# Kernel tuning notes

Hardware: AMD Instinct MI355X
Metric: run time of the kernel (lower is better)

Reference implementation:

```python
import jax, jax.numpy as jnp
import numpy as np


def setup_inputs() -> dict:
    key = jax.random.key(0)
    k1, k2, k3, k4, k5 = jax.random.split(key, 5)
    N, E, C_in, C_out = 100000, 1600000, 64, 64
    x = jax.random.normal(k1, (N, C_in), dtype=jnp.float32)
    edge_index = jax.random.randint(k2, (2, E), 0, N, dtype=jnp.int64)
    edge_weight = jax.random.uniform(k3, (E,), dtype=jnp.float32)
    # Xavier-uniform Linear weights [out, in], zero biases (matches reset_parameters)
    bound = float(np.sqrt(6.0 / (C_in + C_out)))
    W_self = jax.random.uniform(k4, (C_out, C_in), dtype=jnp.float32, minval=-bound, maxval=bound)
    W_neigh = jax.random.uniform(k5, (C_out, C_in), dtype=jnp.float32, minval=-bound, maxval=bound)
    b_self = jnp.zeros((C_out,), dtype=jnp.float32)
    b_neigh = jnp.zeros((C_out,), dtype=jnp.float32)
    return {"x": x, "edge_index": edge_index, "edge_weight": edge_weight,
            "W_self": W_self, "b_self": b_self, "W_neigh": W_neigh, "b_neigh": b_neigh,
            "num_nodes": N}


def reference(x, edge_index, edge_weight, W_self, b_self, W_neigh, b_neigh, num_nodes):
    row, col = edge_index[0], edge_index[1]
    # gather source features, weight, scatter-add to destinations: [E, C] -> [N, C]
    message = x[col] * edge_weight[:, None]
    neigh_agg = jax.ops.segment_sum(message, row, num_segments=num_nodes)
    # two linear projections (torch Linear: y = x @ W.T + b)
    return x @ W_self.T + b_self + neigh_agg @ W_neigh.T + b_neigh
```

## Files before the change

### kernel.cpp

```cpp
#include <hip/hip_runtime.h>
#include <hip/hip_bf16.h>


#define C 64
#define BKT 128
#define MAXB 800
#define BINT 6144
#define BTHR 1024
#define CAP 2560

typedef __attribute__((ext_vector_type(8))) short bf16x8;
typedef __attribute__((ext_vector_type(4))) float f32x4;

__device__ inline unsigned short f2bf(float f) {
    union { __hip_bfloat16 h; unsigned short u; } c;
    c.h = __float2bfloat16(f);
    return c.u;
}

__device__ inline float bflo16(unsigned int u) {
    return __int_as_float((int)(u << 16));
}
__device__ inline float bfhi16(unsigned int u) {
    return __int_as_float((int)(u & 0xFFFF0000u));
}

__global__ __launch_bounds__(256) void prep_kernel(
        const int* __restrict__ ei, int* __restrict__ bhist, int E, int NBK,
        const float* __restrict__ x, unsigned short* __restrict__ xb, int n4,
        const float* __restrict__ Ws, const float* __restrict__ Wn,
        unsigned short* __restrict__ Wsb, unsigned short* __restrict__ Wnb) {
    __shared__ int lh[MAXB];
    const int t = threadIdx.x;
    for (int i = t; i < NBK; i += 256) lh[i] = 0;
    __syncthreads();
    const int gtid = blockIdx.x * 256 + t;
    const int gs = gridDim.x * 256;
    for (int e = gtid; e < E; e += gs)
        atomicAdd(&lh[ei[e] >> 7], 1);
    __syncthreads();
    for (int i = t; i < NBK; i += 256)
        if (lh[i]) atomicAdd(&bhist[i], lh[i]);
    const float4* x4 = (const float4*)x;
    ushort4* xb4 = (ushort4*)xb;
    for (int i = gtid; i < n4; i += gs) {
        float4 v = x4[i];
        ushort4 o;
        o.x = f2bf(v.x); o.y = f2bf(v.y); o.z = f2bf(v.z); o.w = f2bf(v.w);
        xb4[i] = o;
    }
    if (gtid < 1024) {
        float4 v = ((const float4*)Ws)[gtid];
        ushort4 o;
        o.x = f2bf(v.x); o.y = f2bf(v.y); o.z = f2bf(v.z); o.w = f2bf(v.w);
        ((ushort4*)Wsb)[gtid] = o;
        v = ((const float4*)Wn)[gtid];
        o.x = f2bf(v.x); o.y = f2bf(v.y); o.z = f2bf(v.z); o.w = f2bf(v.w);
        ((ushort4*)Wnb)[gtid] = o;
    }
}

__global__ __launch_bounds__(1024) void scan_kernel(
        const int* __restrict__ bhist, int* __restrict__ boffs,
        int* __restrict__ bcur, int NBK) {
    __shared__ int s[1024];
    const int t = threadIdx.x;
    s[t] = (t < NBK) ? bhist[t] : 0;
    __syncthreads();
    for (int off = 1; off < 1024; off <<= 1) {
        int v = 0;
        if (t >= off) v = s[t - off];
        __syncthreads();
        if (t >= off) s[t] += v;
        __syncthreads();
    }
    if (t < NBK) {
        int e = (t > 0) ? s[t - 1] : 0;
        boffs[t] = e;
        bcur[t] = e;
        if (t == NBK - 1) boffs[NBK] = s[t];
    }
}

__global__ __launch_bounds__(BTHR) void bin_kernel(
        const int* __restrict__ ei, const float* __restrict__ ew,
        int* __restrict__ bcur, const int* __restrict__ unused,
        int2* __restrict__ sorted, int E, int NBK) {
    __shared__ int2 stage[BINT];
    __shared__ unsigned short stageb[BINT];
    __shared__ int h[MAXB];
    __shared__ int cur[MAXB];
    __shared__ int adj[MAXB];
    __shared__ int wsum[16];

    const int t = threadIdx.x;
    const int lane = t & 63;
    const int wv = t >> 6;
    const int e0 = blockIdx.x * BINT;
    const int cnt = min(BINT, E - e0);

    for (int i = t; i < NBK; i += BTHR) h[i] = 0;
    __syncthreads();

#pragma unroll
    for (int k = 0; k < BINT / BTHR; ++k) {
        const int idx = t + k * BTHR;
        if (idx < cnt) atomicAdd(&h[ei[e0 + idx] >> 7], 1);
    }
    __syncthreads();

    const int val = (t < NBK) ? h[t] : 0;
    int v = val;
#pragma unroll
    for (int off = 1; off < 64; off <<= 1) {
        const int u = __shfl_up(v, off);
        if (lane >= off) v += u;
    }
    if (lane == 63) wsum[wv] = v;
    __syncthreads();
    if (t < 64) {
        int s = (lane < 16) ? wsum[lane] : 0;
#pragma unroll
        for (int off = 1; off < 16; off <<= 1) {
            const int u = __shfl_up(s, off);
            if (lane >= off) s += u;
        }
        if (lane < 16) wsum[lane] = s;
    }
    __syncthreads();
    if (t < NBK) {
        const int incl = v + ((wv > 0) ? wsum[wv - 1] : 0);
        const int excl = incl - val;
        cur[t] = excl;
        const int g = val ? atomicAdd(&bcur[t], val) : 0;
        adj[t] = g - excl;
    }
    __syncthreads();

#pragma unroll
    for (int k = 0; k < BINT / BTHR; ++k) {
        const int idx = t + k * BTHR;
        if (idx < cnt) {
            const int e = e0 + idx;
            const int d = ei[e];
            const int s = ei[E + e];
            const float w = ew[e];
            const int b = d >> 7;
            const int dl = d & 127;
            const int p = atomicAdd(&cur[b], 1);
            stage[p] = make_int2((dl << 17) | s, __float_as_int(w));
            stageb[p] = (unsigned short)b;
        }
    }
    __syncthreads();

    for (int i = t; i < cnt; i += BTHR) {
        const int b = stageb[i];
        sorted[adj[b] + i] = stage[i];
    }
}

__global__ __launch_bounds__(512) void agg_kernel(
        const unsigned short* __restrict__ xb,
        const int2* __restrict__ sorted,
        const int* __restrict__ boffs,
        float* __restrict__ agg,
        unsigned short* __restrict__ aggb,
        int N) {
    __shared__ int2 meta2[CAP];
    __shared__ int lcnt[BKT];
    __shared__ int lincl[BKT];
    __shared__ int lcur[BKT];

    const int t = threadIdx.x;
    const int b = blockIdx.x;
    const int node0 = b << 7;
    const int lane = t & 63;
    const int wv = t >> 6;
    const int oct = lane >> 3;
    const int co = lane & 7;

    const bool h1 = (lane & 8) != 0;
    const bool h2 = (lane & 16) != 0;
    const bool h3 = (lane & 32) != 0;
    const int ch = co * 8 + (h1 ? 4 : 0) + (h2 ? 2 : 0) + (h3 ? 1 : 0);

    const uint4* xb8 = (const uint4*)xb;

    const int beg = boffs[b];
    const int end = boffs[b + 1];

    int chunk = beg;
    do {
        const int cc = (end - chunk < CAP) ? (end - chunk) : CAP;

        for (int i = t; i < BKT; i += 512) lcnt[i] = 0;
        __syncthreads();

        for (int i = t; i < cc; i += 512)
            atomicAdd(&lcnt[sorted[chunk + i].x >> 17], 1);
        __syncthreads();

        if (t < BKT) lincl[t] = lcnt[t];
        __syncthreads();
        for (int off = 1; off < BKT; off <<= 1) {
            int v = 0;
            if (t < BKT && t >= off) v = lincl[t - off];
            __syncthreads();
            if (t < BKT && t >= off) lincl[t] += v;
            __syncthreads();
        }
        if (t < BKT) lcur[t] = lincl[t] - lcnt[t];
        __syncthreads();

        for (int i = t; i < cc; i += 512) {
            const int2 m = sorted[chunk + i];
            const int dl = m.x >> 17;
            const int p = atomicAdd(&lcur[dl], 1);
            meta2[p] = make_int2(m.x & 0x1FFFF, m.y);
        }
        __syncthreads();

        const bool first = (chunk == beg);
        const bool last = (chunk + CAP >= end);

        for (int r = wv; r < BKT; r += 8) {
            const int s1 = lincl[r];
            const int s0 = s1 - lcnt[r];
            float a0 = 0.f, a1 = 0.f, a2 = 0.f, a3 = 0.f;
            float a4 = 0.f, a5 = 0.f, a6 = 0.f, a7 = 0.f;
            int j = s0 + oct;
            for (; j + 8 < s1; j += 16) {
                const int2 m0 = meta2[j];
                const int2 m1 = meta2[j + 8];
                const uint4 u0 = xb8[(unsigned)m0.x * 8u + co];
                const uint4 u1 = xb8[(unsigned)m1.x * 8u + co];
                const float w0 = __int_as_float(m0.y);
                const float w1 = __int_as_float(m1.y);
                a0 += w0 * bflo16(u0.x); a1 += w0 * bfhi16(u0.x);
                a2 += w0 * bflo16(u0.y); a3 += w0 * bfhi16(u0.y);
                a4 += w0 * bflo16(u0.z); a5 += w0 * bfhi16(u0.z);
                a6 += w0 * bflo16(u0.w); a7 += w0 * bfhi16(u0.w);
                a0 += w1 * bflo16(u1.x); a1 += w1 * bfhi16(u1.x);
                a2 += w1 * bflo16(u1.y); a3 += w1 * bfhi16(u1.y);
                a4 += w1 * bflo16(u1.z); a5 += w1 * bfhi16(u1.z);
                a6 += w1 * bflo16(u1.w); a7 += w1 * bfhi16(u1.w);
            }
            if (j < s1) {
                const int2 m0 = meta2[j];
                const uint4 u0 = xb8[(unsigned)m0.x * 8u + co];
                const float w0 = __int_as_float(m0.y);
                a0 += w0 * bflo16(u0.x); a1 += w0 * bfhi16(u0.x);
                a2 += w0 * bflo16(u0.y); a3 += w0 * bfhi16(u0.y);
                a4 += w0 * bflo16(u0.z); a5 += w0 * bfhi16(u0.z);
                a6 += w0 * bflo16(u0.w); a7 += w0 * bfhi16(u0.w);
            }
            float r0 = __shfl_xor(h1 ? a0 : a4, 8);
            float r1 = __shfl_xor(h1 ? a1 : a5, 8);
            float r2 = __shfl_xor(h1 ? a2 : a6, 8);
            float r3 = __shfl_xor(h1 ? a3 : a7, 8);
            const float b0 = (h1 ? a4 : a0) + r0;
            const float b1 = (h1 ? a5 : a1) + r1;
            const float b2 = (h1 ? a6 : a2) + r2;
            const float b3 = (h1 ? a7 : a3) + r3;
            float r4 = __shfl_xor(h2 ? b0 : b2, 16);
            float r5 = __shfl_xor(h2 ? b1 : b3, 16);
            const float c0 = (h2 ? b2 : b0) + r4;
            const float c1 = (h2 ? b3 : b1) + r5;
            float r6 = __shfl_xor(h3 ? c0 : c1, 32);
            float vfin = (h3 ? c1 : c0) + r6;

            const int node = node0 + r;
            if (node < N) {
                const size_t off = (size_t)node * C + ch;
                if (last) {
                    if (!first) vfin += agg[off];
                    aggb[off] = f2bf(vfin);
                } else {
                    if (first) agg[off] = vfin;
                    else       agg[off] += vfin;
                }
            }
        }
        chunk += CAP;
        __syncthreads();
    } while (chunk < end);
}

__global__ __launch_bounds__(256) void scatter_kernel(
        const float* __restrict__ x, const int* __restrict__ ei,
        const float* __restrict__ ew, float* __restrict__ agg, int E) {
    const int lane = threadIdx.x & 63;
    const int wid = (blockIdx.x * blockDim.x + threadIdx.x) >> 6;
    const int nw = (gridDim.x * blockDim.x) >> 6;
    for (int base = wid * 64; base < E; base += nw * 64) {
        const int e = base + lane;
        int dst = 0, src = 0; float w = 0.f;
        if (e < E) { dst = ei[e]; src = ei[E + e]; w = ew[e]; }
        const int cnt = min(64, E - base);
        for (int j = 0; j < cnt; ++j) {
            const int d = __shfl(dst, j);
            const int s = __shfl(src, j);
            const float wj = __shfl(w, j);
            atomicAdd(&agg[d * C + lane], x[s * C + lane] * wj);
        }
    }
}

__device__ inline bf16x8 cvt8(const float* __restrict__ p) {
    f32x4 lo = *(const f32x4*)p;
    f32x4 hi = *(const f32x4*)(p + 4);
    union { bf16x8 v; __hip_bfloat16 e[8]; } u;
#pragma unroll
    for (int j = 0; j < 4; ++j) u.e[j] = __float2bfloat16(lo[j]);
#pragma unroll
    for (int j = 0; j < 4; ++j) u.e[4 + j] = __float2bfloat16(hi[j]);
    return u.v;
}

__global__ __launch_bounds__(256) void proj_kernel(
        const float* __restrict__ x, const float* __restrict__ agg,
        const float* __restrict__ Ws, const float* __restrict__ bs,
        const float* __restrict__ Wn, const float* __restrict__ bn,
        float* __restrict__ out, int N) {
    const int lane = threadIdx.x & 63;
    const int wid = (blockIdx.x * blockDim.x + threadIdx.x) >> 6;
    const int l15 = lane & 15;
    const int quad = lane >> 4;
    const int nTiles = N >> 4;
    if (wid >= nTiles) return;
    const int m0 = wid << 4;

    bf16x8 bsf[4][2], bnf[4][2];
#pragma unroll
    for (int tt = 0; tt < 4; ++tt) {
        const int o = tt * 16 + l15;
#pragma unroll
        for (int h = 0; h < 2; ++h) {
            bsf[tt][h] = cvt8(Ws + o * C + h * 32 + quad * 8);
            bnf[tt][h] = cvt8(Wn + o * C + h * 32 + quad * 8);
        }
    }

    const int m = m0 + l15;
    bf16x8 ax[2], ag[2];
#pragma unroll
    for (int h = 0; h < 2; ++h) {
        ax[h] = cvt8(x + m * C + h * 32 + quad * 8);
        ag[h] = cvt8(agg + m * C + h * 32 + quad * 8);
    }

#pragma unroll
    for (int tt = 0; tt < 4; ++tt) {
        f32x4 acc = {0.f, 0.f, 0.f, 0.f};
        acc = __builtin_amdgcn_mfma_f32_16x16x32_bf16(ax[0], bsf[tt][0], acc, 0, 0, 0);
        acc = __builtin_amdgcn_mfma_f32_16x16x32_bf16(ax[1], bsf[tt][1], acc, 0, 0, 0);
        acc = __builtin_amdgcn_mfma_f32_16x16x32_bf16(ag[0], bnf[tt][0], acc, 0, 0, 0);
        acc = __builtin_amdgcn_mfma_f32_16x16x32_bf16(ag[1], bnf[tt][1], acc, 0, 0, 0);
        const int o = tt * 16 + l15;
        const float bias = bs[o] + bn[o];
#pragma unroll
        for (int r = 0; r < 4; ++r)
            out[(m0 + quad * 4 + r) * C + o] = acc[r] + bias;
    }
}

__global__ __launch_bounds__(256) void projb_kernel(
        const unsigned short* __restrict__ xb,
        const unsigned short* __restrict__ aggb,
        const unsigned short* __restrict__ Wsb, const float* __restrict__ bs,
        const unsigned short* __restrict__ Wnb, const float* __restrict__ bn,
        float* __restrict__ out, int N) {
    const int lane = threadIdx.x & 63;
    const int wid = (blockIdx.x * blockDim.x + threadIdx.x) >> 6;
    const int l15 = lane & 15;
    const int quad = lane >> 4;
    const int nTiles = N >> 4;
    if (wid >= nTiles) return;
    const int m0 = wid << 4;

    bf16x8 bsf[4][2], bnf[4][2];
#pragma unroll
    for (int tt = 0; tt < 4; ++tt) {
        const int o = tt * 16 + l15;
#pragma unroll
        for (int h = 0; h < 2; ++h) {
            bsf[tt][h] = *(const bf16x8*)(Wsb + o * C + h * 32 + quad * 8);
            bnf[tt][h] = *(const bf16x8*)(Wnb + o * C + h * 32 + quad * 8);
        }
    }

    const int m = m0 + l15;
    bf16x8 ax[2], ag[2];
#pragma unroll
    for (int h = 0; h < 2; ++h) {
        ax[h] = *(const bf16x8*)(xb + (size_t)m * C + h * 32 + quad * 8);
        ag[h] = *(const bf16x8*)(aggb + (size_t)m * C + h * 32 + quad * 8);
    }

#pragma unroll
    for (int tt = 0; tt < 4; ++tt) {
        f32x4 acc = {0.f, 0.f, 0.f, 0.f};
        acc = __builtin_amdgcn_mfma_f32_16x16x32_bf16(ax[0], bsf[tt][0], acc, 0, 0, 0);
        acc = __builtin_amdgcn_mfma_f32_16x16x32_bf16(ax[1], bsf[tt][1], acc, 0, 0, 0);
        acc = __builtin_amdgcn_mfma_f32_16x16x32_bf16(ag[0], bnf[tt][0], acc, 0, 0, 0);
        acc = __builtin_amdgcn_mfma_f32_16x16x32_bf16(ag[1], bnf[tt][1], acc, 0, 0, 0);
        const int o = tt * 16 + l15;
        const float bias = bs[o] + bn[o];
#pragma unroll
        for (int r = 0; r < 4; ++r)
            out[(m0 + quad * 4 + r) * C + o] = acc[r] + bias;
    }
}

extern "C" void kernel_launch(void* const* d_in, const int* in_sizes, int n_in,
                              void* d_out, int out_size, void* d_ws, size_t ws_size,
                              hipStream_t stream) {
    const float* x  = (const float*)d_in[0];
    const int*   ei = (const int*)d_in[1];
    const float* ew = (const float*)d_in[2];
    const float* Ws = (const float*)d_in[3];
    const float* bs = (const float*)d_in[4];
    const float* Wn = (const float*)d_in[5];
    const float* bn = (const float*)d_in[6];

    const int N = in_sizes[0] / C;
    const int E = in_sizes[2];
    const int NBK = (N + BKT - 1) / BKT;

    char* p = (char*)d_ws;
    float* agg = (float*)p;                  p += (size_t)N * C * sizeof(float);
    unsigned short* xb = (unsigned short*)p;  p += (size_t)N * C * sizeof(short);
    unsigned short* aggb = (unsigned short*)p; p += (size_t)N * C * sizeof(short);
    int2* sorted = (int2*)p;                 p += (size_t)E * sizeof(int2);
    unsigned short* Wsb = (unsigned short*)p; p += (size_t)C * C * sizeof(short);
    unsigned short* Wnb = (unsigned short*)p; p += (size_t)C * C * sizeof(short);
    int* bhist = (int*)p;                    p += (size_t)MAXB * sizeof(int);
    int* boffs = (int*)p;                    p += (size_t)(MAXB + 1) * sizeof(int);
    int* bcur = (int*)p;                     p += (size_t)MAXB * sizeof(int);
    const size_t needed = (size_t)(p - (char*)d_ws);

    const int nTiles = N / 16;
    const int projBlocks = (nTiles + 3) / 4;

    if (needed <= ws_size && N <= (1 << 17) && NBK <= MAXB) {
        const int n4 = N * C / 4;
        hipMemsetAsync(bhist, 0, (size_t)NBK * sizeof(int), stream);
        prep_kernel<<<1024, 256, 0, stream>>>(ei, bhist, E, NBK, x, xb, n4,
                                              Ws, Wn, Wsb, Wnb);
        scan_kernel<<<1, 1024, 0, stream>>>(bhist, boffs, bcur, NBK);
        bin_kernel<<<(E + BINT - 1) / BINT, BTHR, 0, stream>>>(ei, ew, bcur, bhist,
                                                               sorted, E, NBK);
        agg_kernel<<<NBK, 512, 0, stream>>>(xb, sorted, boffs, agg, aggb, N);
        projb_kernel<<<projBlocks, 256, 0, stream>>>(xb, aggb, Wsb, bs, Wnb, bn,
                                                     (float*)d_out, N);
    } else {
        hipMemsetAsync(agg, 0, (size_t)N * C * sizeof(float), stream);
        scatter_kernel<<<2048, 256, 0, stream>>>(x, ei, ew, agg, E);
        proj_kernel<<<projBlocks, 256, 0, stream>>>(x, agg, Ws, bs, Wn, bn,
                                                    (float*)d_out, N);
    }
}
```

Measured before the change: 194.5 us.

## Fuse projection into aggregation kernel and move bf16 conversion into bin kernel

The projection GEMM now runs inside agg_kernel: each block writes its aggregated bf16 rows into a swizzled LDS tile and applies MFMA projections directly. This drops the aggb buffer round trip and one kernel launch. The x/weight bf16 conversion moves from prep_kernel to the tail of bin_kernel, and the agg per-chunk scan uses wave shuffles instead of a barrier-heavy LDS scan. The extra 16KB LDS tile may lower agg_kernel occupancy, and weights are now read from global memory per tile.

```diff
diff --git a/kernel.cpp b/kernel.cpp
--- a/kernel.cpp
+++ b/kernel.cpp
@@ -26,10 +26,7 @@
 }
 
 __global__ __launch_bounds__(256) void prep_kernel(
-        const int* __restrict__ ei, int* __restrict__ bhist, int E, int NBK,
-        const float* __restrict__ x, unsigned short* __restrict__ xb, int n4,
-        const float* __restrict__ Ws, const float* __restrict__ Wn,
-        unsigned short* __restrict__ Wsb, unsigned short* __restrict__ Wnb) {
+        const int* __restrict__ ei, int* __restrict__ bhist, int E, int NBK) {
     __shared__ int lh[MAXB];
     const int t = threadIdx.x;
     for (int i = t; i < NBK; i += 256) lh[i] = 0;
@@ -41,23 +38,6 @@
     __syncthreads();
     for (int i = t; i < NBK; i += 256)
         if (lh[i]) atomicAdd(&bhist[i], lh[i]);
-    const float4* x4 = (const float4*)x;
-    ushort4* xb4 = (ushort4*)xb;
-    for (int i = gtid; i < n4; i += gs) {
-        float4 v = x4[i];
-        ushort4 o;
-        o.x = f2bf(v.x); o.y = f2bf(v.y); o.z = f2bf(v.z); o.w = f2bf(v.w);
-        xb4[i] = o;
-    }
-    if (gtid < 1024) {
-        float4 v = ((const float4*)Ws)[gtid];
-        ushort4 o;
-        o.x = f2bf(v.x); o.y = f2bf(v.y); o.z = f2bf(v.z); o.w = f2bf(v.w);
-        ((ushort4*)Wsb)[gtid] = o;
-        v = ((const float4*)Wn)[gtid];
-        o.x = f2bf(v.x); o.y = f2bf(v.y); o.z = f2bf(v.z); o.w = f2bf(v.w);
-        ((ushort4*)Wnb)[gtid] = o;
-    }
 }
 
 __global__ __launch_bounds__(1024) void scan_kernel(
@@ -84,8 +64,11 @@
 
 __global__ __launch_bounds__(BTHR) void bin_kernel(
         const int* __restrict__ ei, const float* __restrict__ ew,
-        int* __restrict__ bcur, const int* __restrict__ unused,
-        int2* __restrict__ sorted, int E, int NBK) {
+        int* __restrict__ bcur,
+        int2* __restrict__ sorted, int E, int NBK,
+        const float* __restrict__ x, unsigned short* __restrict__ xb, int n4,
+        const float* __restrict__ Ws, const float* __restrict__ Wn,
+        unsigned short* __restrict__ Wsb, unsigned short* __restrict__ Wnb) {
     __shared__ int2 stage[BINT];
     __shared__ unsigned short stageb[BINT];
     __shared__ int h[MAXB];
@@ -158,6 +141,26 @@
         const int b = stageb[i];
         sorted[adj[b] + i] = stage[i];
     }
+
+    const int gtid = blockIdx.x * BTHR + t;
+    const int gs = gridDim.x * BTHR;
+    const float4* x4 = (const float4*)x;
+    ushort4* xb4 = (ushort4*)xb;
+    for (int i = gtid; i < n4; i += gs) {
+        float4 vv = x4[i];
+        ushort4 o;
+        o.x = f2bf(vv.x); o.y = f2bf(vv.y); o.z = f2bf(vv.z); o.w = f2bf(vv.w);
+        xb4[i] = o;
+    }
+    if (gtid < 1024) {
+        float4 vv = ((const float4*)Ws)[gtid];
+        ushort4 o;
+        o.x = f2bf(vv.x); o.y = f2bf(vv.y); o.z = f2bf(vv.z); o.w = f2bf(vv.w);
+        ((ushort4*)Wsb)[gtid] = o;
+        vv = ((const float4*)Wn)[gtid];
+        o.x = f2bf(vv.x); o.y = f2bf(vv.y); o.z = f2bf(vv.z); o.w = f2bf(vv.w);
+        ((ushort4*)Wnb)[gtid] = o;
+    }
 }
 
 __global__ __launch_bounds__(512) void agg_kernel(
@@ -165,12 +168,14 @@
         const int2* __restrict__ sorted,
         const int* __restrict__ boffs,
         float* __restrict__ agg,
-        unsigned short* __restrict__ aggb,
-        int N) {
+        const unsigned short* __restrict__ Wsb, const float* __restrict__ bs,
+        const unsigned short* __restrict__ Wnb, const float* __restrict__ bn,
+        float* __restrict__ out, int N) {
     __shared__ int2 meta2[CAP];
     __shared__ int lcnt[BKT];
     __shared__ int lincl[BKT];
     __shared__ int lcur[BKT];
+    __shared__ unsigned short tile[BKT * C];
 
     const int t = threadIdx.x;
     const int b = blockIdx.x;
@@ -179,6 +184,8 @@
     const int wv = t >> 6;
     const int oct = lane >> 3;
     const int co = lane & 7;
+    const int l15 = lane & 15;
+    const int quad = lane >> 4;
 
     const bool h1 = (lane & 8) != 0;
     const bool h2 = (lane & 16) != 0;
@@ -201,15 +208,19 @@
             atomicAdd(&lcnt[sorted[chunk + i].x >> 17], 1);
         __syncthreads();
 
-        if (t < BKT) lincl[t] = lcnt[t];
-        __syncthreads();
-        for (int off = 1; off < BKT; off <<= 1) {
-            int v = 0;
-            if (t < BKT && t >= off) v = lincl[t - off];
-            __syncthreads();
-            if (t < BKT && t >= off) lincl[t] += v;
-            __syncthreads();
-        }
+        if (t < BKT) {
+            int sv = lcnt[t];
+            int acc = sv;
+#pragma unroll
+            for (int off = 1; off < 64; off <<= 1) {
+                const int u = __shfl_up(acc, off);
+                if (lane >= off) acc += u;
+            }
+            lincl[t] = acc;
+        }
+        __syncthreads();
+        if (t >= 64 && t < BKT) lincl[t] += lincl[63];
+        __syncthreads();
         if (t < BKT) lcur[t] = lincl[t] - lcnt[t];
         __syncthreads();
 
@@ -271,17 +282,53 @@
             float vfin = (h3 ? c1 : c0) + r6;
 
             const int node = node0 + r;
-            if (node < N) {
-                const size_t off = (size_t)node * C + ch;
-                if (last) {
-                    if (!first) vfin += agg[off];
-                    aggb[off] = f2bf(vfin);
-                } else {
-                    if (first) agg[off] = vfin;
-                    else       agg[off] += vfin;
+            const size_t off = (size_t)node * C + ch;
+            if (last) {
+                if (!first && node < N) vfin += agg[off];
+                const int idx = r * C + ((((ch >> 3) ^ (r & 7)) << 3) | (ch & 7));
+                tile[idx] = f2bf(vfin);
+            } else if (node < N) {
+                if (first) agg[off] = vfin;
+                else       agg[off] += vfin;
+            }
+        }
+
+        if (last) {
+            __syncthreads();
+            const int ml = (wv << 4) + l15;
+            const int node = node0 + ml;
+            const int nclamp = (node < N) ? node : 0;
+
+            bf16x8 ax[2], ag[2];
+#pragma unroll
+            for (int hh = 0; hh < 2; ++hh) {
+                const int slot = (hh * 4 + quad) ^ (ml & 7);
+                ag[hh] = *(const bf16x8*)&tile[ml * C + slot * 8];
+                ax[hh] = *(const bf16x8*)(xb + (size_t)nclamp * C + hh * 32 + quad * 8);
+            }
+
+#pragma unroll
+            for (int tt = 0; tt < 4; ++tt) {
+                const int o = tt * 16 + l15;
+                f32x4 acc = {0.f, 0.f, 0.f, 0.f};
+                acc = __builtin_amdgcn_mfma_f32_16x16x32_bf16(
+                        ax[0], *(const bf16x8*)(Wsb + o * C + quad * 8), acc, 0, 0, 0);
+                acc = __builtin_amdgcn_mfma_f32_16x16x32_bf16(
+                        ax[1], *(const bf16x8*)(Wsb + o * C + 32 + quad * 8), acc, 0, 0, 0);
+                acc = __builtin_amdgcn_mfma_f32_16x16x32_bf16(
+                        ag[0], *(const bf16x8*)(Wnb + o * C + quad * 8), acc, 0, 0, 0);
+                acc = __builtin_amdgcn_mfma_f32_16x16x32_bf16(
+                        ag[1], *(const bf16x8*)(Wnb + o * C + 32 + quad * 8), acc, 0, 0, 0);
+                const float bias = bs[o] + bn[o];
+#pragma unroll
+                for (int rr = 0; rr < 4; ++rr) {
+                    const int orow = node0 + (wv << 4) + quad * 4 + rr;
+                    if (orow < N)
+                        out[(size_t)orow * C + o] = acc[rr] + bias;
                 }
             }
         }
+
         chunk += CAP;
         __syncthreads();
     } while (chunk < end);
@@ -365,54 +412,6 @@
     }
 }
 
-__global__ __launch_bounds__(256) void projb_kernel(
-        const unsigned short* __restrict__ xb,
-        const unsigned short* __restrict__ aggb,
-        const unsigned short* __restrict__ Wsb, const float* __restrict__ bs,
-        const unsigned short* __restrict__ Wnb, const float* __restrict__ bn,
-        float* __restrict__ out, int N) {
-    const int lane = threadIdx.x & 63;
-    const int wid = (blockIdx.x * blockDim.x + threadIdx.x) >> 6;
-    const int l15 = lane & 15;
-    const int quad = lane >> 4;
-    const int nTiles = N >> 4;
-    if (wid >= nTiles) return;
-    const int m0 = wid << 4;
-
-    bf16x8 bsf[4][2], bnf[4][2];
-#pragma unroll
-    for (int tt = 0; tt < 4; ++tt) {
-        const int o = tt * 16 + l15;
-#pragma unroll
-        for (int h = 0; h < 2; ++h) {
-            bsf[tt][h] = *(const bf16x8*)(Wsb + o * C + h * 32 + quad * 8);
-            bnf[tt][h] = *(const bf16x8*)(Wnb + o * C + h * 32 + quad * 8);
-        }
-    }
-
-    const int m = m0 + l15;
-    bf16x8 ax[2], ag[2];
-#pragma unroll
-    for (int h = 0; h < 2; ++h) {
-        ax[h] = *(const bf16x8*)(xb + (size_t)m * C + h * 32 + quad * 8);
-        ag[h] = *(const bf16x8*)(aggb + (size_t)m * C + h * 32 + quad * 8);
-    }
-
-#pragma unroll
-    for (int tt = 0; tt < 4; ++tt) {
-        f32x4 acc = {0.f, 0.f, 0.f, 0.f};
-        acc = __builtin_amdgcn_mfma_f32_16x16x32_bf16(ax[0], bsf[tt][0], acc, 0, 0, 0);
-        acc = __builtin_amdgcn_mfma_f32_16x16x32_bf16(ax[1], bsf[tt][1], acc, 0, 0, 0);
-        acc = __builtin_amdgcn_mfma_f32_16x16x32_bf16(ag[0], bnf[tt][0], acc, 0, 0, 0);
-        acc = __builtin_amdgcn_mfma_f32_16x16x32_bf16(ag[1], bnf[tt][1], acc, 0, 0, 0);
-        const int o = tt * 16 + l15;
-        const float bias = bs[o] + bn[o];
-#pragma unroll
-        for (int r = 0; r < 4; ++r)
-            out[(m0 + quad * 4 + r) * C + o] = acc[r] + bias;
-    }
-}
-
 extern "C" void kernel_launch(void* const* d_in, const int* in_sizes, int n_in,
                               void* d_out, int out_size, void* d_ws, size_t ws_size,
                               hipStream_t stream) {
@@ -431,7 +430,6 @@
     char* p = (char*)d_ws;
     float* agg = (float*)p;                  p += (size_t)N * C * sizeof(float);
     unsigned short* xb = (unsigned short*)p;  p += (size_t)N * C * sizeof(short);
-    unsigned short* aggb = (unsigned short*)p; p += (size_t)N * C * sizeof(short);
     int2* sorted = (int2*)p;                 p += (size_t)E * sizeof(int2);
     unsigned short* Wsb = (unsigned short*)p; p += (size_t)C * C * sizeof(short);
     unsigned short* Wnb = (unsigned short*)p; p += (size_t)C * C * sizeof(short);
@@ -440,21 +438,19 @@
     int* bcur = (int*)p;                     p += (size_t)MAXB * sizeof(int);
     const size_t needed = (size_t)(p - (char*)d_ws);
 
-    const int nTiles = N / 16;
-    const int projBlocks = (nTiles + 3) / 4;
-
     if (needed <= ws_size && N <= (1 << 17) && NBK <= MAXB) {
         const int n4 = N * C / 4;
         hipMemsetAsync(bhist, 0, (size_t)NBK * sizeof(int), stream);
-        prep_kernel<<<1024, 256, 0, stream>>>(ei, bhist, E, NBK, x, xb, n4,
-                                              Ws, Wn, Wsb, Wnb);
+        prep_kernel<<<1024, 256, 0, stream>>>(ei, bhist, E, NBK);
         scan_kernel<<<1, 1024, 0, stream>>>(bhist, boffs, bcur, NBK);
-        bin_kernel<<<(E + BINT - 1) / BINT, BTHR, 0, stream>>>(ei, ew, bcur, bhist,
-                                                               sorted, E, NBK);
-        agg_kernel<<<NBK, 512, 0, stream>>>(xb, sorted, boffs, agg, aggb, N);
-        projb_kernel<<<projBlocks, 256, 0, stream>>>(xb, aggb, Wsb, bs, Wnb, bn,
-                                                     (float*)d_out, N);
+        bin_kernel<<<(E + BINT - 1) / BINT, BTHR, 0, stream>>>(
+                ei, ew, bcur, sorted, E, NBK, x, xb, n4, Ws, Wn, Wsb, Wnb);
+        agg_kernel<<<NBK, 512, 0, stream>>>(xb, sorted, boffs, agg,
+                                            Wsb, bs, Wnb, bn,
+                                            (float*)d_out, N);
     } else {
+        const int nTiles = N / 16;
+        const int projBlocks = (nTiles + 3) / 4;
         hipMemsetAsync(agg, 0, (size_t)N * C * sizeof(float), stream);
         scatter_kernel<<<2048, 256, 0, stream>>>(x, ei, ew, agg, E);
         proj_kernel<<<projBlocks, 256, 0, stream>>>(x, agg, Ws, bs, Wn, bn,
```

Result: slower. 203.8 us (+4.8%).
